# Optimization experiments

Hardware: AMD Instinct MI355X
Metric: run time of the kernel (lower is better)

## Reference

```python
import jax, jax.numpy as jnp
import numpy as np

N_NODES = 100000
N_EDGES = 1200000
NODE_IN = 64
EDGE_IN = 32
HIDDEN = 64


def _glorot(key, shape):
    fan_in, fan_out = shape[0], shape[1]
    s = jnp.sqrt(2.0 / (fan_in + fan_out))
    return jax.random.normal(key, shape, dtype=jnp.float32) * s


def setup_inputs() -> dict:
    key = jax.random.key(0)
    ks = jax.random.split(key, 16)
    inp = {
        "x": jax.random.normal(ks[0], (N_NODES, NODE_IN), dtype=jnp.float32),
        "edge_index": jax.random.randint(ks[1], (2, N_EDGES), 0, N_NODES, dtype=jnp.int64),
        "edge_attr": jax.random.normal(ks[2], (N_EDGES, EDGE_IN), dtype=jnp.float32),
        # SAGE layer 0 (in=NODE_IN -> HIDDEN): lin_l (neighbors, has bias), lin_r (root)
        "w_l0": _glorot(ks[3], (NODE_IN, HIDDEN)),
        "w_r0": _glorot(ks[4], (NODE_IN, HIDDEN)),
        "b0": jnp.zeros((HIDDEN,), jnp.float32),
        "ln_g0": jnp.ones((HIDDEN,), jnp.float32),
        "ln_b0": jnp.zeros((HIDDEN,), jnp.float32),
        # SAGE layer 1 (HIDDEN -> HIDDEN)
        "w_l1": _glorot(ks[5], (HIDDEN, HIDDEN)),
        "w_r1": _glorot(ks[6], (HIDDEN, HIDDEN)),
        "b1": jnp.zeros((HIDDEN,), jnp.float32),
        "ln_g1": jnp.ones((HIDDEN,), jnp.float32),
        "ln_b1": jnp.zeros((HIDDEN,), jnp.float32),
        # Edge classifier MLP: in_dim = 3*HIDDEN + EDGE_IN = 224
        "cw1": _glorot(ks[7], (3 * HIDDEN + EDGE_IN, HIDDEN)),
        "cb1": jnp.zeros((HIDDEN,), jnp.float32),
        "cw2": _glorot(ks[8], (HIDDEN, HIDDEN // 2)),
        "cb2": jnp.zeros((HIDDEN // 2,), jnp.float32),
        "cw3": _glorot(ks[9], (HIDDEN // 2, 1)),
        "cb3": jnp.zeros((1,), jnp.float32),
    }
    return inp


def _sage_conv(x, src, dst, w_l, w_r, b):
    # mean-aggregate source features at destination nodes (PyG SAGEConv, aggr='mean')
    n = x.shape[0]
    msg = x[src]  # [E, F] gather
    agg = jax.ops.segment_sum(msg, dst, num_segments=n)
    cnt = jax.ops.segment_sum(jnp.ones((src.shape[0], 1), x.dtype), dst, num_segments=n)
    mean = agg / jnp.maximum(cnt, 1.0)
    return mean @ w_l + x @ w_r + b


def _layer_norm(x, g, b, eps=1e-5):
    mu = jnp.mean(x, axis=-1, keepdims=True)
    var = jnp.var(x, axis=-1, keepdims=True)
    return (x - mu) * jax.lax.rsqrt(var + eps) * g + b


def reference(x, edge_index, edge_attr,
              w_l0, w_r0, b0, ln_g0, ln_b0,
              w_l1, w_r1, b1, ln_g1, ln_b1,
              cw1, cb1, cw2, cb2, cw3, cb3):
    src, dst = edge_index[0], edge_index[1]
    # Encoder (eval mode: dropout is identity)
    h = jax.nn.relu(_layer_norm(_sage_conv(x, src, dst, w_l0, w_r0, b0), ln_g0, ln_b0))
    z = jax.nn.relu(_layer_norm(_sage_conv(h, src, dst, w_l1, w_r1, b1), ln_g1, ln_b1))
    # Edge classifier: gather-concat-MLP
    z_src = z[src]
    z_dst = z[dst]
    edge_repr = jnp.concatenate([z_src, z_dst, z_src * z_dst, edge_attr], axis=-1)
    h1 = jax.nn.relu(edge_repr @ cw1 + cb1)
    h2 = jax.nn.relu(h1 @ cw2 + cb2)
    logits = (h2 @ cw3 + cb3).squeeze(-1)  # [E]
    return logits
```

## Files before the change

kernel.cpp:

```cpp
#include <hip/hip_runtime.h>
#include <hip/hip_bf16.h>

#define N_NODES 100000
#define N_EDGES 1200000

typedef __attribute__((ext_vector_type(8))) short bfrag;
typedef __attribute__((ext_vector_type(4))) float ffrag;

union FragU { uint4 v; uint32_t u[4]; bfrag f; };

__device__ __forceinline__ ushort bfbits(float a) {
  union { __hip_bfloat16 h; ushort u; } c; c.h = __float2bfloat16(a); return c.u;
}
__device__ __forceinline__ uint32_t pkbf(float a, float b) {
  union { __hip_bfloat162 h; uint32_t u; } c;
  c.h = __float22bfloat162_rn(float2{a, b}); return c.u;
}
__device__ __forceinline__ uint32_t mul2bf(uint32_t a, uint32_t b) {
  union { uint32_t u; __hip_bfloat162 h; } x, y, r;
  x.u = a; y.u = b; r.h = __hmul2(x.h, y.h); return r.u;
}
__device__ __forceinline__ float bflo(uint32_t u) { return __int_as_float(u << 16); }
__device__ __forceinline__ float bfhi(uint32_t u) { return __int_as_float(u & 0xffff0000u); }

template <int CTRL>
__device__ __forceinline__ float dpp_add16(float v) {
  int x = __builtin_amdgcn_update_dpp(0, __float_as_int(v), CTRL, 0xF, 0xF, true);
  return v + __int_as_float(x);
}
__device__ __forceinline__ float reduce16(float v) {
  v = dpp_add16<0xB1>(v);
  v = dpp_add16<0x4E>(v);
  v = dpp_add16<0x141>(v);
  v = dpp_add16<0x140>(v);
  return v;
}


__global__ void cvt_k(const float* __restrict__ x, ushort* __restrict__ xb, int n2) {
  int i = blockIdx.x * blockDim.x + threadIdx.x;
  if (i < n2) {
    float2 v = ((const float2*)x)[i];
    ((uint32_t*)xb)[i] = pkbf(v.x, v.y);
  }
}


__global__ void hist_k(const int* __restrict__ ei, int* __restrict__ deg,
                       int* __restrict__ rank, int E) {
  int e = blockIdx.x * blockDim.x + threadIdx.x;
  if (e < E) rank[e] = atomicAdd(&deg[ei[E + e]], 1);
}

__global__ __launch_bounds__(1024) void scan1_k(const int* __restrict__ deg,
                                                int* __restrict__ off,
                                                int* __restrict__ bsum, int n) {
  __shared__ int wpart[16];
  __shared__ int wpre[16];
  int tid = threadIdx.x, lane = tid & 63, wid = tid >> 6;
  int i = blockIdx.x * 1024 + tid;
  int v = (i < n) ? deg[i] : 0;
  int x = v;
  #pragma unroll
  for (int o = 1; o < 64; o <<= 1) {
    int y = __shfl_up(x, o);
    if (lane >= o) x += y;
  }
  if (lane == 63) wpart[wid] = x;
  __syncthreads();
  if (tid == 0) {
    int run = 0;
    #pragma unroll
    for (int w = 0; w < 16; w++) { int t = wpart[w]; wpre[w] = run; run += t; }
    bsum[blockIdx.x] = run;
  }
  __syncthreads();
  if (i < n) off[i] = x - v + wpre[wid];
}

__global__ void scan2_k(const int* __restrict__ bsum, int* __restrict__ bpre,
                        int* __restrict__ off, int nb, int n) {
  if (threadIdx.x == 0) {
    int run = 0;
    for (int b = 0; b < nb; b++) { int t = bsum[b]; bpre[b] = run; run += t; }
    off[n] = run;
  }
}

__global__ __launch_bounds__(1024) void scan3_k(int* __restrict__ off,
                                                const int* __restrict__ bpre, int n) {
  int i = blockIdx.x * 1024 + threadIdx.x;
  if (i < n) off[i] += bpre[blockIdx.x];
}

__global__ void fill_k(const int* __restrict__ ei, const int* __restrict__ off,
                       const int* __restrict__ rank, int* __restrict__ csr, int E) {
  int e = blockIdx.x * blockDim.x + threadIdx.x;
  if (e < E) {
    int d = ei[E + e];
    int p = off[d] + rank[e];
    __builtin_nontemporal_store(ei[e], &csr[p]);
  }
}


__global__ __launch_bounds__(256) void agg_k(
    const ushort* __restrict__ Xb, const int* __restrict__ off, const int* __restrict__ csr,
    ushort* __restrict__ aggout, int n) {
  int lane = threadIdx.x & 63;
  int quad = lane >> 4, f8 = lane & 15;
  int wave = blockIdx.x * 4 + (threadIdx.x >> 6);
  int nw = gridDim.x * 4;
  int nquads = (n + 3) >> 2;
  const uint2* X2 = (const uint2*)Xb;
  for (int p = wave; p < nquads; p += nw) {
    int i = p * 4 + quad;
    int ic = i < n ? i : n - 1;
    int s0 = off[ic], s1 = off[ic + 1];
    float a0 = 0.f, a1 = 0.f, a2 = 0.f, a3 = 0.f;
    for (int j = s0; j < s1; j += 8) {
      int id[8]; uint2 us[8];
      #pragma unroll
      for (int u = 0; u < 8; u++) {
        int jj = j + u;
        id[u] = csr[jj < s1 ? jj : s1 - 1];
      }
      #pragma unroll
      for (int u = 0; u < 8; u++) us[u] = X2[(size_t)id[u] * 16 + f8];
      #pragma unroll
      for (int u = 0; u < 8; u++) {
        if (j + u < s1) {
          a0 += bflo(us[u].x); a1 += bfhi(us[u].x);
          a2 += bflo(us[u].y); a3 += bfhi(us[u].y);
        }
      }
    }
    if (i < n) {
      float rdeg = 1.f / fmaxf((float)(s1 - s0), 1.f);
      uint2 w;
      w.x = pkbf(a0 * rdeg, a1 * rdeg);
      w.y = pkbf(a2 * rdeg, a3 * rdeg);
      ((uint2*)aggout)[(size_t)i * 16 + f8] = w;
    }
  }
}


__global__ __launch_bounds__(256) void node_k(
    const ushort* __restrict__ agg, const ushort* __restrict__ selfb,
    const float* __restrict__ wl, const float* __restrict__ wr,
    const float* __restrict__ bias, const float* __restrict__ g, const float* __restrict__ lb,
    ushort* __restrict__ outb, int n) {
  __shared__ ushort wt[64 * 128];
  const int tid = threadIdx.x;
  for (int i = tid; i < 8192; i += 256) {
    int k = i >> 6, nn = i & 63;
    float v = (k < 64) ? wl[k * 64 + nn] : wr[(k - 64) * 64 + nn];
    wt[nn * 128 + (((k >> 3) ^ (nn & 7)) * 8) + (k & 7)] = bfbits(v);
  }
  __syncthreads();
  const int lane = tid & 63, wid = tid >> 6;
  const int ln = lane & 15, q = lane >> 4;
  float bias_n[4], g_n[4], lb_n[4];
  #pragma unroll
  for (int nt = 0; nt < 4; nt++) {
    bias_n[nt] = bias[nt * 16 + ln];
    g_n[nt] = g[nt * 16 + ln];
    lb_n[nt] = lb[nt * 16 + ln];
  }
  const int ntiles = (n + 15) >> 4;
  for (int t = blockIdx.x * 4 + wid; t < ntiles; t += gridDim.x * 4) {
    int node = t * 16 + ln;
    int nc = node < n ? node : n - 1;
    FragU afr[4];
    #pragma unroll
    for (int kk = 0; kk < 2; kk++) {
      afr[kk].v     = ((const uint4*)agg)[(size_t)nc * 8 + kk * 4 + q];
      afr[2 + kk].v = ((const uint4*)selfb)[(size_t)nc * 8 + kk * 4 + q];
    }
    ffrag acc[4];
    #pragma unroll
    for (int nt = 0; nt < 4; nt++) acc[nt] = ffrag{0.f, 0.f, 0.f, 0.f};
    #pragma unroll
    for (int kk = 0; kk < 4; kk++) {
      bfrag a = afr[kk].f;
      #pragma unroll
      for (int nt = 0; nt < 4; nt++) {
        int nn = nt * 16 + ln;
        int b = kk * 4 + q;
        const bfrag* bp = (const bfrag*)&wt[nn * 128 + ((b ^ (nn & 7)) * 8)];
        acc[nt] = __builtin_amdgcn_mfma_f32_16x16x32_bf16(a, *bp, acc[nt], 0, 0, 0);
      }
    }
    #pragma unroll
    for (int r = 0; r < 4; r++) {
      int m = t * 16 + q * 4 + r;
      float o[4];
      #pragma unroll
      for (int nt = 0; nt < 4; nt++) o[nt] = acc[nt][r] + bias_n[nt];
      float s = (o[0] + o[1]) + (o[2] + o[3]);
      #pragma unroll
      for (int mm = 1; mm < 16; mm <<= 1) s += __shfl_xor(s, mm);
      float mu = s * (1.f / 64.f);
      float v2 = 0.f;
      #pragma unroll
      for (int nt = 0; nt < 4; nt++) { float d2 = o[nt] - mu; v2 += d2 * d2; }
      #pragma unroll
      for (int mm = 1; mm < 16; mm <<= 1) v2 += __shfl_xor(v2, mm);
      float rs = rsqrtf(v2 * (1.f / 64.f) + 1e-5f);
      if (m < n) {
        #pragma unroll
        for (int nt = 0; nt < 4; nt++) {
          float y = fmaxf((o[nt] - mu) * rs * g_n[nt] + lb_n[nt], 0.f);
          outb[(size_t)m * 64 + nt * 16 + ln] = bfbits(y);
        }
      }
    }
  }
}


__global__ __launch_bounds__(256, 2) void edge_mfma_k(
    const int* __restrict__ ei, const float* __restrict__ ea,
    const ushort* __restrict__ zb,
    const float* __restrict__ cw1, const float* __restrict__ cb1,
    const float* __restrict__ cw2, const float* __restrict__ cb2,
    const float* __restrict__ cw3, const float* __restrict__ cb3,
    float* __restrict__ out, int E) {
  __shared__ ushort smem[64 * 256];
  const int tid = threadIdx.x;

  for (int i = tid; i < 224 * 64; i += 256) {
    int k = i >> 6, n = i & 63;
    int blk = k >> 3;
    smem[n * 256 + ((blk ^ (n & 7)) * 8) + (k & 7)] = bfbits(cw1[i]);
  }
  __syncthreads();

  const int lane = tid & 63, wid = tid >> 6;
  const int ln = lane & 15, q = lane >> 4;

  FragU w1f[7][4];
  #pragma unroll
  for (int kk = 0; kk < 7; kk++) {
    #pragma unroll
    for (int tt = 0; tt < 4; tt++) {
      int n = tt * 16 + ln;
      int b = kk * 4 + q;
      w1f[kk][tt].v = *(const uint4*)&smem[n * 256 + ((b ^ (n & 7)) * 8)];
    }
  }
  __syncthreads();
  ushort* hb = &smem[wid * 1024];

  float cb1v[4];
  #pragma unroll
  for (int t = 0; t < 4; t++) cb1v[t] = cb1[t * 16 + ln];
  float cb2a = cb2[ln], cb2b = cb2[16 + ln];
  float w3a = cw3[ln], w3b = cw3[16 + ln];
  float cb3v = cb3[0];

  FragU w2f[2][2];
  #pragma unroll
  for (int t2 = 0; t2 < 2; t2++) {
    #pragma unroll
    for (int kk = 0; kk < 2; kk++) {
      #pragma unroll
      for (int p = 0; p < 4; p++) {
        int k = kk * 32 + q * 8 + p * 2;
        int n = t2 * 16 + ln;
        w2f[t2][kk].u[p] = pkbf(cw2[k * 32 + n], cw2[(k + 1) * 32 + n]);
      }
    }
  }

  const int nt = E >> 4;
  const int S = gridDim.x * 4;
  int t = blockIdx.x * 4 + wid;
  if (t >= nt) return;

  FragU curz[4]; uint32_t cea[4];
  {
    int e = t * 16 + ln;
    int s = ei[e], d = ei[E + e];
    curz[0].v = ((const uint4*)zb)[(size_t)s * 8 + q];
    curz[1].v = ((const uint4*)zb)[(size_t)s * 8 + 4 + q];
    curz[2].v = ((const uint4*)zb)[(size_t)d * 8 + q];
    curz[3].v = ((const uint4*)zb)[(size_t)d * 8 + 4 + q];
    float4 l0 = ((const float4*)ea)[(size_t)e * 8 + q * 2];
    float4 l1 = ((const float4*)ea)[(size_t)e * 8 + q * 2 + 1];
    cea[0] = pkbf(l0.x, l0.y); cea[1] = pkbf(l0.z, l0.w);
    cea[2] = pkbf(l1.x, l1.y); cea[3] = pkbf(l1.z, l1.w);
  }

  for (; t < nt; t += S) {
    int tn = t + S;
    int tc = tn < nt ? tn : t;
    FragU nz[4]; uint32_t nea[4];
    {
      int e = tc * 16 + ln;
      int s = ei[e], d = ei[E + e];
      nz[0].v = ((const uint4*)zb)[(size_t)s * 8 + q];
      nz[1].v = ((const uint4*)zb)[(size_t)s * 8 + 4 + q];
      nz[2].v = ((const uint4*)zb)[(size_t)d * 8 + q];
      nz[3].v = ((const uint4*)zb)[(size_t)d * 8 + 4 + q];
      float4 l0 = ((const float4*)ea)[(size_t)e * 8 + q * 2];
      float4 l1 = ((const float4*)ea)[(size_t)e * 8 + q * 2 + 1];
      nea[0] = pkbf(l0.x, l0.y); nea[1] = pkbf(l0.z, l0.w);
      nea[2] = pkbf(l1.x, l1.y); nea[3] = pkbf(l1.z, l1.w);
    }

    ffrag acc1[4];
    #pragma unroll
    for (int tt = 0; tt < 4; tt++) acc1[tt] = ffrag{0.f, 0.f, 0.f, 0.f};
    #pragma unroll
    for (int kk = 0; kk < 7; kk++) {
      FragU af;
      if (kk < 4) af = curz[kk];
      else if (kk < 6) {
        #pragma unroll
        for (int p = 0; p < 4; p++) af.u[p] = mul2bf(curz[kk - 4].u[p], curz[kk - 2].u[p]);
      } else {
        #pragma unroll
        for (int p = 0; p < 4; p++) af.u[p] = cea[p];
      }
      bfrag a = af.f;
      #pragma unroll
      for (int tt = 0; tt < 4; tt++)
        acc1[tt] = __builtin_amdgcn_mfma_f32_16x16x32_bf16(a, w1f[kk][tt].f, acc1[tt], 0, 0, 0);
    }

    #pragma unroll
    for (int tt = 0; tt < 4; tt++) {
      #pragma unroll
      for (int r = 0; r < 4; r++) {
        int m = q * 4 + r;
        int col = tt * 16 + ln;
        float v = fmaxf(acc1[tt][r] + cb1v[tt], 0.f);
        hb[m * 64 + (((col >> 3) ^ (m & 7)) * 8) + (col & 7)] = bfbits(v);
      }
    }

    ffrag acc2[2];
    acc2[0] = ffrag{0.f, 0.f, 0.f, 0.f};
    acc2[1] = ffrag{0.f, 0.f, 0.f, 0.f};
    #pragma unroll
    for (int kk = 0; kk < 2; kk++) {
      int b = kk * 4 + q;
      const bfrag* ap = (const bfrag*)&hb[ln * 64 + ((b ^ (ln & 7)) * 8)];
      bfrag a2 = *ap;
      acc2[0] = __builtin_amdgcn_mfma_f32_16x16x32_bf16(a2, w2f[0][kk].f, acc2[0], 0, 0, 0);
      acc2[1] = __builtin_amdgcn_mfma_f32_16x16x32_bf16(a2, w2f[1][kk].f, acc2[1], 0, 0, 0);
    }

    float p0 = fmaxf(acc2[0][0] + cb2a, 0.f) * w3a + fmaxf(acc2[1][0] + cb2b, 0.f) * w3b;
    float p1 = fmaxf(acc2[0][1] + cb2a, 0.f) * w3a + fmaxf(acc2[1][1] + cb2b, 0.f) * w3b;
    float p2 = fmaxf(acc2[0][2] + cb2a, 0.f) * w3a + fmaxf(acc2[1][2] + cb2b, 0.f) * w3b;
    float p3 = fmaxf(acc2[0][3] + cb2a, 0.f) * w3a + fmaxf(acc2[1][3] + cb2b, 0.f) * w3b;
    p0 = reduce16(p0); p1 = reduce16(p1); p2 = reduce16(p2); p3 = reduce16(p3);
    float keep = (ln == 0) ? p0 : (ln == 1) ? p1 : (ln == 2) ? p2 : p3;
    if (ln < 4) out[t * 16 + q * 4 + ln] = keep + cb3v;

    curz[0] = nz[0]; curz[1] = nz[1]; curz[2] = nz[2]; curz[3] = nz[3];
    cea[0] = nea[0]; cea[1] = nea[1]; cea[2] = nea[2]; cea[3] = nea[3];
  }
}


extern "C" void kernel_launch(void* const* d_in, const int* in_sizes, int n_in,
                              void* d_out, int out_size, void* d_ws, size_t ws_size,
                              hipStream_t stream) {
  const float* x   = (const float*)d_in[0];
  const int*   ei  = (const int*)d_in[1];
  const float* ea  = (const float*)d_in[2];
  const float* wl0 = (const float*)d_in[3];
  const float* wr0 = (const float*)d_in[4];
  const float* b0  = (const float*)d_in[5];
  const float* g0  = (const float*)d_in[6];
  const float* lb0 = (const float*)d_in[7];
  const float* wl1 = (const float*)d_in[8];
  const float* wr1 = (const float*)d_in[9];
  const float* b1  = (const float*)d_in[10];
  const float* g1  = (const float*)d_in[11];
  const float* lb1 = (const float*)d_in[12];
  const float* cw1 = (const float*)d_in[13];
  const float* cb1 = (const float*)d_in[14];
  const float* cw2 = (const float*)d_in[15];
  const float* cb2 = (const float*)d_in[16];
  const float* cw3 = (const float*)d_in[17];
  const float* cb3 = (const float*)d_in[18];
  float* out = (float*)d_out;
  const int N = N_NODES, E = N_EDGES;
  const int NB = (N + 1023) / 1024;

  uintptr_t pp = (uintptr_t)d_ws;
  auto alloc = [&](size_t bytes) {
    uintptr_t r = (pp + 255) & ~(uintptr_t)255; pp = r + bytes; return (void*)r;
  };
  int* deg  = (int*)alloc((size_t)N * 4);
  int* off  = (int*)alloc((size_t)(N + 1) * 4);
  int* rank = (int*)alloc((size_t)E * 4);
  int* csr  = (int*)alloc((size_t)E * 4);
  int* bsum = (int*)alloc((size_t)NB * 4);
  int* bpre = (int*)alloc((size_t)NB * 4);
  ushort* xb  = (ushort*)alloc((size_t)N * 64 * 2);
  ushort* agg = (ushort*)alloc((size_t)N * 64 * 2);
  ushort* hb  = (ushort*)alloc((size_t)N * 64 * 2);
  ushort* zb  = (ushort*)alloc((size_t)N * 64 * 2);

  hipMemsetAsync(deg, 0, (size_t)N * 4, stream);
  cvt_k<<<(N * 32 + 255) / 256, 256, 0, stream>>>(x, xb, N * 32);
  hist_k<<<(E + 255) / 256, 256, 0, stream>>>(ei, deg, rank, E);
  scan1_k<<<NB, 1024, 0, stream>>>(deg, off, bsum, N);
  scan2_k<<<1, 64, 0, stream>>>(bsum, bpre, off, NB, N);
  scan3_k<<<NB, 1024, 0, stream>>>(off, bpre, N);
  fill_k<<<(E + 255) / 256, 256, 0, stream>>>(ei, off, rank, csr, E);
  agg_k<<<2048, 256, 0, stream>>>(xb, off, csr, agg, N);
  node_k<<<512, 256, 0, stream>>>(agg, xb, wl0, wr0, b0, g0, lb0, hb, N);
  agg_k<<<2048, 256, 0, stream>>>(hb, off, csr, agg, N);
  node_k<<<512, 256, 0, stream>>>(agg, hb, wl1, wr1, b1, g1, lb1, zb, N);
  edge_mfma_k<<<512, 256, 0, stream>>>(ei, ea, zb, cw1, cb1, cw2, cb2, cw3, cb3, out, E);
}
```

Measured before the change: 509.4 us.

## Triple-buffer edge gathers with deeper prefetch and nontemporal loads in edge MLP

The edge classifier kernel now keeps three in-flight tiles of gathered z features and prefetches edge indices two stages ahead, issuing the next gathers between the first and second MLP layers. This is meant to hide the latency of random gathers. It also moves the cw2 fragments from registers into shared memory to free VGPRs for the extra buffers, and marks streaming loads and stores as nontemporal across several kernels. The cost is more register pressure, extra LDS reads per tile, and some redundant clamped work at the tail.

```diff
diff --git a/kernel.cpp b/kernel.cpp
--- a/kernel.cpp
+++ b/kernel.cpp
@@ -6,6 +6,7 @@
 
 typedef __attribute__((ext_vector_type(8))) short bfrag;
 typedef __attribute__((ext_vector_type(4))) float ffrag;
+typedef __attribute__((ext_vector_type(4))) float nf4;
 
 union FragU { uint4 v; uint32_t u[4]; bfrag f; };
 
@@ -40,8 +41,9 @@
 __global__ void cvt_k(const float* __restrict__ x, ushort* __restrict__ xb, int n2) {
   int i = blockIdx.x * blockDim.x + threadIdx.x;
   if (i < n2) {
-    float2 v = ((const float2*)x)[i];
-    ((uint32_t*)xb)[i] = pkbf(v.x, v.y);
+    float a = __builtin_nontemporal_load(x + i * 2);
+    float b = __builtin_nontemporal_load(x + i * 2 + 1);
+    ((uint32_t*)xb)[i] = pkbf(a, b);
   }
 }
 
@@ -123,7 +125,7 @@
       #pragma unroll
       for (int u = 0; u < 8; u++) {
         int jj = j + u;
-        id[u] = csr[jj < s1 ? jj : s1 - 1];
+        id[u] = __builtin_nontemporal_load(csr + (jj < s1 ? jj : s1 - 1));
       }
       #pragma unroll
       for (int u = 0; u < 8; u++) us[u] = X2[(size_t)id[u] * 16 + f8];
@@ -228,6 +230,7 @@
     const float* __restrict__ cw3, const float* __restrict__ cb3,
     float* __restrict__ out, int E) {
   __shared__ ushort smem[64 * 256];
+  __shared__ ushort ws2[2048];
   const int tid = threadIdx.x;
 
   for (int i = tid; i < 224 * 64; i += 256) {
@@ -248,6 +251,22 @@
       int n = tt * 16 + ln;
       int b = kk * 4 + q;
       w1f[kk][tt].v = *(const uint4*)&smem[n * 256 + ((b ^ (n & 7)) * 8)];
+    }
+  }
+  if (wid == 0) {
+    #pragma unroll
+    for (int t2 = 0; t2 < 2; t2++) {
+      #pragma unroll
+      for (int kk = 0; kk < 2; kk++) {
+        uint32_t w[4];
+        #pragma unroll
+        for (int p = 0; p < 4; p++) {
+          int k = kk * 32 + q * 8 + p * 2;
+          int n = t2 * 16 + ln;
+          w[p] = pkbf(cw2[k * 32 + n], cw2[(k + 1) * 32 + n]);
+        }
+        *(uint4*)&ws2[((t2 * 2 + kk) * 64 + lane) * 8] = make_uint4(w[0], w[1], w[2], w[3]);
+      }
     }
   }
   __syncthreads();
@@ -260,55 +279,38 @@
   float w3a = cw3[ln], w3b = cw3[16 + ln];
   float cb3v = cb3[0];
 
-  FragU w2f[2][2];
-  #pragma unroll
-  for (int t2 = 0; t2 < 2; t2++) {
-    #pragma unroll
-    for (int kk = 0; kk < 2; kk++) {
-      #pragma unroll
-      for (int p = 0; p < 4; p++) {
-        int k = kk * 32 + q * 8 + p * 2;
-        int n = t2 * 16 + ln;
-        w2f[t2][kk].u[p] = pkbf(cw2[k * 32 + n], cw2[(k + 1) * 32 + n]);
-      }
-    }
-  }
-
   const int nt = E >> 4;
   const int S = gridDim.x * 4;
-  int t = blockIdx.x * 4 + wid;
-  if (t >= nt) return;
-
-  FragU curz[4]; uint32_t cea[4];
-  {
-    int e = t * 16 + ln;
-    int s = ei[e], d = ei[E + e];
-    curz[0].v = ((const uint4*)zb)[(size_t)s * 8 + q];
-    curz[1].v = ((const uint4*)zb)[(size_t)s * 8 + 4 + q];
-    curz[2].v = ((const uint4*)zb)[(size_t)d * 8 + q];
-    curz[3].v = ((const uint4*)zb)[(size_t)d * 8 + 4 + q];
-    float4 l0 = ((const float4*)ea)[(size_t)e * 8 + q * 2];
-    float4 l1 = ((const float4*)ea)[(size_t)e * 8 + q * 2 + 1];
-    cea[0] = pkbf(l0.x, l0.y); cea[1] = pkbf(l0.z, l0.w);
-    cea[2] = pkbf(l1.x, l1.y); cea[3] = pkbf(l1.z, l1.w);
-  }
-
-  for (; t < nt; t += S) {
-    int tn = t + S;
-    int tc = tn < nt ? tn : t;
-    FragU nz[4]; uint32_t nea[4];
-    {
-      int e = tc * 16 + ln;
-      int s = ei[e], d = ei[E + e];
-      nz[0].v = ((const uint4*)zb)[(size_t)s * 8 + q];
-      nz[1].v = ((const uint4*)zb)[(size_t)s * 8 + 4 + q];
-      nz[2].v = ((const uint4*)zb)[(size_t)d * 8 + q];
-      nz[3].v = ((const uint4*)zb)[(size_t)d * 8 + 4 + q];
-      float4 l0 = ((const float4*)ea)[(size_t)e * 8 + q * 2];
-      float4 l1 = ((const float4*)ea)[(size_t)e * 8 + q * 2 + 1];
-      nea[0] = pkbf(l0.x, l0.y); nea[1] = pkbf(l0.z, l0.w);
-      nea[2] = pkbf(l1.x, l1.y); nea[3] = pkbf(l1.z, l1.w);
-    }
+  const int S3 = 3 * S;
+  const int w0 = blockIdx.x * 4 + wid;
+  const uint4* Z4 = (const uint4*)zb;
+  const nf4* EA4 = (const nf4*)ea;
+
+  FragU zA[4], zB[4], zC[4];
+  int svA, dvA, svB, dvB, svC, dvC;
+
+  auto prol = [&](FragU (&z)[4], int &sv, int &dv, int u) {
+    int uc = u < nt ? u : nt - 1;
+    int e = uc * 16 + ln;
+    int s = __builtin_nontemporal_load(ei + e);
+    int d = __builtin_nontemporal_load(ei + E + e);
+    z[0].v = Z4[(size_t)s * 8 + q];
+    z[1].v = Z4[(size_t)s * 8 + 4 + q];
+    z[2].v = Z4[(size_t)d * 8 + q];
+    z[3].v = Z4[(size_t)d * 8 + 4 + q];
+    int un = u + S3 < nt ? u + S3 : nt - 1;
+    sv = __builtin_nontemporal_load(ei + un * 16 + ln);
+    dv = __builtin_nontemporal_load(ei + E + un * 16 + ln);
+  };
+  prol(zA, svA, dvA, w0);
+  prol(zB, svB, dvB, w0 + S);
+  prol(zC, svC, dvC, w0 + 2 * S);
+
+  auto half = [&](FragU (&z)[4], int &sv, int &dv, int u) {
+    int uc = u < nt ? u : nt - 1;
+    int e = uc * 16 + ln;
+    nf4 l0 = __builtin_nontemporal_load(EA4 + (size_t)e * 8 + q * 2);
+    nf4 l1 = __builtin_nontemporal_load(EA4 + (size_t)e * 8 + q * 2 + 1);
 
     ffrag acc1[4];
     #pragma unroll
@@ -316,18 +318,28 @@
     #pragma unroll
     for (int kk = 0; kk < 7; kk++) {
       FragU af;
-      if (kk < 4) af = curz[kk];
+      if (kk < 4) af = z[kk];
       else if (kk < 6) {
         #pragma unroll
-        for (int p = 0; p < 4; p++) af.u[p] = mul2bf(curz[kk - 4].u[p], curz[kk - 2].u[p]);
+        for (int p = 0; p < 4; p++) af.u[p] = mul2bf(z[kk - 4].u[p], z[kk - 2].u[p]);
       } else {
-        #pragma unroll
-        for (int p = 0; p < 4; p++) af.u[p] = cea[p];
+        af.u[0] = pkbf(l0.x, l0.y); af.u[1] = pkbf(l0.z, l0.w);
+        af.u[2] = pkbf(l1.x, l1.y); af.u[3] = pkbf(l1.z, l1.w);
       }
       bfrag a = af.f;
       #pragma unroll
       for (int tt = 0; tt < 4; tt++)
         acc1[tt] = __builtin_amdgcn_mfma_f32_16x16x32_bf16(a, w1f[kk][tt].f, acc1[tt], 0, 0, 0);
+    }
+
+    {
+      z[0].v = Z4[(size_t)sv * 8 + q];
+      z[1].v = Z4[(size_t)sv * 8 + 4 + q];
+      z[2].v = Z4[(size_t)dv * 8 + q];
+      z[3].v = Z4[(size_t)dv * 8 + 4 + q];
+      int uf = u + 2 * S3 < nt ? u + 2 * S3 : nt - 1;
+      sv = __builtin_nontemporal_load(ei + uf * 16 + ln);
+      dv = __builtin_nontemporal_load(ei + E + uf * 16 + ln);
     }
 
     #pragma unroll
@@ -349,8 +361,10 @@
       int b = kk * 4 + q;
       const bfrag* ap = (const bfrag*)&hb[ln * 64 + ((b ^ (ln & 7)) * 8)];
       bfrag a2 = *ap;
-      acc2[0] = __builtin_amdgcn_mfma_f32_16x16x32_bf16(a2, w2f[0][kk].f, acc2[0], 0, 0, 0);
-      acc2[1] = __builtin_amdgcn_mfma_f32_16x16x32_bf16(a2, w2f[1][kk].f, acc2[1], 0, 0, 0);
+      const bfrag* b0p = (const bfrag*)&ws2[((0 * 2 + kk) * 64 + lane) * 8];
+      const bfrag* b1p = (const bfrag*)&ws2[((1 * 2 + kk) * 64 + lane) * 8];
+      acc2[0] = __builtin_amdgcn_mfma_f32_16x16x32_bf16(a2, *b0p, acc2[0], 0, 0, 0);
+      acc2[1] = __builtin_amdgcn_mfma_f32_16x16x32_bf16(a2, *b1p, acc2[1], 0, 0, 0);
     }
 
     float p0 = fmaxf(acc2[0][0] + cb2a, 0.f) * w3a + fmaxf(acc2[1][0] + cb2b, 0.f) * w3b;
@@ -359,10 +373,14 @@
     float p3 = fmaxf(acc2[0][3] + cb2a, 0.f) * w3a + fmaxf(acc2[1][3] + cb2b, 0.f) * w3b;
     p0 = reduce16(p0); p1 = reduce16(p1); p2 = reduce16(p2); p3 = reduce16(p3);
     float keep = (ln == 0) ? p0 : (ln == 1) ? p1 : (ln == 2) ? p2 : p3;
-    if (ln < 4) out[t * 16 + q * 4 + ln] = keep + cb3v;
-
-    curz[0] = nz[0]; curz[1] = nz[1]; curz[2] = nz[2]; curz[3] = nz[3];
-    cea[0] = nea[0]; cea[1] = nea[1]; cea[2] = nea[2]; cea[3] = nea[3];
+    if (u < nt && ln < 4)
+      __builtin_nontemporal_store(keep + cb3v, &out[u * 16 + q * 4 + ln]);
+  };
+
+  for (int t = w0; t < nt; t += S3) {
+    half(zA, svA, dvA, t);
+    half(zB, svB, dvB, t + S);
+    half(zC, svC, dvC, t + 2 * S);
   }
 }
 
```

Measured after the change: 503.4 us. Within noise of the previous version (-1.2%).
